# Optimization experiments

Hardware: AMD Instinct MI355X
Metric: run time of the kernel (lower is better)

Reference implementation:

```python
import jax, jax.numpy as jnp
import numpy as np
from jax import lax

B, C_IN, H_IN, W_IN = 128, 256, 8, 32
RH, RW = 16, 64            # rec-head resolution
YOH, XOH = RH // 2, RW // 2  # onehot sizes (8, 32)
HID = 256
NC = 163                   # num classes == embed size
T = 32                     # target length
C_ENC = C_IN + XOH + YOH   # 296 encoder channels
L = (RH // 2) * (RW // 2)  # 256 attention positions


def setup_inputs() -> dict:
    key = jax.random.key(0)
    ks = jax.random.split(key, 18)
    s = 0.05
    return {
        "x": jax.random.normal(ks[0], (B, C_IN, H_IN, W_IN), jnp.float32),
        "decoder_targets": jax.random.randint(ks[1], (B, T), 0, NC),
        "word_targets": jax.random.randint(ks[2], (B, T), 0, NC),
        # seq_encoder conv 3x3
        "conv_w": jax.random.normal(ks[3], (C_IN, C_IN, 3, 3), jnp.float32) * 0.02,
        "conv_b": jnp.zeros((C_IN,), jnp.float32),
        # decoder embedding (post kaiming re-init => random, not identity)
        "emb_dec": jax.random.normal(ks[4], (NC, NC), jnp.float32) * s,
        "word_w": jax.random.normal(ks[5], (HID, NC), jnp.float32) * s,
        "word_b": jnp.zeros((HID,), jnp.float32),
        "attn_w": jax.random.normal(ks[6], (HID, 2 * HID + XOH + YOH), jnp.float32) * s,
        "attn_b": jnp.zeros((HID,), jnp.float32),
        "attn_v": jax.random.normal(ks[7], (HID,), jnp.float32) * (1.0 / np.sqrt(HID)),
        # GRUCell, gate order [r, z, n]
        "gru_wih": jax.random.normal(ks[8], (3 * HID, 2 * HID + XOH + YOH), jnp.float32) * s,
        "gru_bih": jnp.zeros((3 * HID,), jnp.float32),
        "gru_whh": jax.random.normal(ks[9], (3 * HID, HID), jnp.float32) * s,
        "gru_bhh": jnp.zeros((3 * HID,), jnp.float32),
        "out_w": jax.random.normal(ks[10], (NC, HID), jnp.float32) * s,
        "out_b": jnp.zeros((NC,), jnp.float32),
        # positional one-hot embedding tables (also kaiming re-initialized)
        "x_emb": jax.random.normal(ks[11], (XOH, XOH), jnp.float32) * s,
        "y_emb": jax.random.normal(ks[12], (YOH, YOH), jnp.float32) * s,
    }


def _forward(x, conv_w, conv_b, emb_dec, word_w, word_b, attn_w, attn_b, attn_v,
             gru_wih, gru_bih, gru_whh, gru_bhh, out_w, out_b, x_emb, y_emb,
             decoder_targets, word_targets):
    b = x.shape[0]
    # rescale: bilinear upsample (align_corners=False ~ half-pixel)
    xr = jax.image.resize(x, (b, C_IN, RH, RW), method="linear")
    # seq_encoder: conv3x3 + ReLU + maxpool2
    conv = lax.conv_general_dilated(xr, conv_w, (1, 1), "SAME",
                                    dimension_numbers=("NCHW", "OIHW", "NCHW"))
    conv = jax.nn.relu(conv + conv_b[None, :, None, None])
    pooled = lax.reduce_window(conv, -jnp.inf, lax.max,
                               (1, 1, 2, 2), (1, 1, 2, 2), "VALID")  # (B,256,8,32)
    hf, wf = RH // 2, RW // 2
    # positional channels: x_map[c,y,x] = x_emb[x,c]; y_map[c,y,x] = y_emb[y,c]
    x_map = jnp.broadcast_to(x_emb.T[:, None, :], (XOH, hf, wf))
    y_map = jnp.broadcast_to(y_emb.T[:, :, None], (YOH, hf, wf))
    x_map = jnp.broadcast_to(x_map[None], (b, XOH, hf, wf))
    y_map = jnp.broadcast_to(y_map[None], (b, YOH, hf, wf))
    feat = jnp.concatenate([pooled, x_map, y_map], axis=1)      # (B,296,8,32)
    enc = feat.reshape(b, C_ENC, hf * wf).transpose(0, 2, 1)    # (B, L, C)

    t_len = decoder_targets.shape[1]
    # teacher forcing: input at step 0 is BOS (=0), else previous target
    inputs_seq = jnp.concatenate(
        [jnp.zeros((b, 1), decoder_targets.dtype), decoder_targets[:, :-1]], axis=1)

    def step(hidden, xs):
        tok, tgt = xs
        we = emb_dec[tok] @ word_w.T + word_b                   # (B, HID)
        # Bahdanau attention
        hrep = jnp.broadcast_to(hidden[:, None, :], (b, enc.shape[1], HID))
        cat = jnp.concatenate([hrep, enc], axis=-1)             # (B,L,2H+OH)
        energy = jnp.tanh(jnp.einsum("blc,hc->blh", cat, attn_w) + attn_b)
        scores = jnp.einsum("blh,h->bl", energy, attn_v)
        w = jax.nn.softmax(scores, axis=1)                      # (B,L)
        ctx = jnp.einsum("bl,blc->bc", w, enc)                  # (B, C)
        rin = jnp.concatenate([we, ctx], axis=-1)               # (B, 2H+OH)
        # GRUCell
        gi = rin @ gru_wih.T + gru_bih
        gh = hidden @ gru_whh.T + gru_bhh
        i_r, i_z, i_n = jnp.split(gi, 3, axis=-1)
        h_r, h_z, h_n = jnp.split(gh, 3, axis=-1)
        r = jax.nn.sigmoid(i_r + h_r)
        z = jax.nn.sigmoid(i_z + h_z)
        n = jnp.tanh(i_n + r * h_n)
        h_new = (1.0 - z) * n + z * hidden
        logp = jax.nn.log_softmax(h_new @ out_w.T + out_b, axis=1)
        # NLLLoss(ignore_index=-1, reduction='none')
        nll = -jnp.take_along_axis(logp, jnp.clip(tgt, 0)[:, None], axis=1)[:, 0]
        nll = jnp.where(tgt >= 0, nll, 0.0)
        return h_new, nll

    h0 = jnp.zeros((b, HID), jnp.float32)
    _, nlls = lax.scan(step, h0, (inputs_seq.T, word_targets.T))  # (T, B)
    loss_vec = nlls.sum(axis=0)                                   # (B,)
    return 0.2 * (loss_vec.sum() / loss_vec.shape[0])


def reference(x, decoder_targets, word_targets, conv_w, conv_b, emb_dec,
              word_w, word_b, attn_w, attn_b, attn_v, gru_wih, gru_bih,
              gru_whh, gru_bhh, out_w, out_b, x_emb, y_emb):
    return _forward(x, conv_w, conv_b, emb_dec, word_w, word_b, attn_w, attn_b,
                    attn_v, gru_wih, gru_bih, gru_whh, gru_bhh, out_w, out_b,
                    x_emb, y_emb, decoder_targets, word_targets)
```

## Files before the change

kernel.cpp:

```cpp
#include <hip/hip_runtime.h>
#include <hip/hip_bf16.h>
#include <math.h>

#define B    128
#define CIN  256
#define HIN  8
#define WIN_ 32
#define RH   16
#define RW   64
#define HID  256
#define NC   163
#define T    32
#define L    256
#define CENC 296

typedef __attribute__((ext_vector_type(8))) short short8;
typedef __attribute__((ext_vector_type(8))) unsigned short u16x8;
typedef __attribute__((ext_vector_type(4))) float f32x4;
typedef unsigned long long u64;

#define PH(k) ((((k) >> 3) * 12) + ((k) & 7))

__device__ __forceinline__ float bf2f(unsigned short u) {
    unsigned int x = ((unsigned int)u) << 16;
    return __uint_as_float(x);
}
__device__ __forceinline__ unsigned short f2bf(float f) {
    unsigned int x = __float_as_uint(f);
    unsigned int r = (x + 0x7FFFu + ((x >> 16) & 1u)) >> 16;
    return (unsigned short)r;
}
__device__ __forceinline__ float fast_tanh(float x) {
    float e = __expf(2.f * x);
    return 1.f - 2.f * __builtin_amdgcn_rcpf(e + 1.f);
}
__device__ __forceinline__ float fast_sigm(float x) {
    return __builtin_amdgcn_rcpf(1.f + __expf(-x));
}
__device__ __forceinline__ float wave_red_max(float v) {
    #pragma unroll
    for (int o = 32; o > 0; o >>= 1) v = fmaxf(v, __shfl_down(v, o, 64));
    return v;
}
__device__ __forceinline__ float wave_red_sum(float v) {
    #pragma unroll
    for (int o = 32; o > 0; o >>= 1) v += __shfl_down(v, o, 64);
    return v;
}
__device__ __forceinline__ float half_red_sum(float v) {
    #pragma unroll
    for (int o = 16; o > 0; o >>= 1) v += __shfl_down(v, o, 64);
    return v;
}

__global__ void __launch_bounds__(256) k_upsxt(const float* __restrict__ x,
                                               unsigned short* __restrict__ Xt) {
    __shared__ __align__(16) float sf[64 * 2 * 32];
    const int y = blockIdx.x;
    const int b = blockIdx.y;
    const int tid = threadIdx.x;
    float sy = 0.5f * y - 0.25f;
    int yq0 = (y - 1) >> 1;
    float wy = sy - (float)yq0;
    int y0c = min(max(yq0, 0), HIN - 1);
    int y1c = min(max(yq0 + 1, 0), HIN - 1);
    const int xo = tid & 63;
    const int cj = tid >> 6;
    float sx = 0.5f * xo - 0.25f;
    int xq0 = (xo - 1) >> 1;
    float wx = sx - (float)xq0;
    int x0c = min(max(xq0, 0), WIN_ - 1);
    int x1c = min(max(xq0 + 1, 0), WIN_ - 1);
    for (int cc = 0; cc < 4; cc++) {
        __syncthreads();
        #pragma unroll
        for (int i = 0; i < 4; i++) {
            int idx = tid * 4 + i;
            int c = idx >> 4;
            int rowh = (idx >> 3) & 1;
            int part = idx & 7;
            int ysrc = rowh ? y1c : y0c;
            float4 v = *reinterpret_cast<const float4*>(
                x + ((size_t)(b * CIN + cc * 64 + c) * HIN + ysrc) * WIN_ + part * 4);
            *reinterpret_cast<float4*>(sf + ((c * 2 + rowh) * 32 + part * 4)) = v;
        }
        __syncthreads();
        unsigned short ov[16];
        #pragma unroll
        for (int j = 0; j < 16; j++) {
            int c = cj * 16 + j;
            const float* r0 = sf + (c * 2 + 0) * 32;
            const float* r1 = sf + (c * 2 + 1) * 32;
            float v = (1.f - wy) * ((1.f - wx) * r0[x0c] + wx * r0[x1c])
                    +        wy  * ((1.f - wx) * r1[x0c] + wx * r1[x1c]);
            ov[j] = f2bf(v);
        }
        unsigned short* dst = Xt + ((size_t)((b * 16 + y) * 64 + xo)) * 256 + cc * 64 + cj * 16;
        *reinterpret_cast<u16x8*>(dst)     = *reinterpret_cast<u16x8*>(ov);
        *reinterpret_cast<u16x8*>(dst + 8) = *reinterpret_cast<u16x8*>(ov + 8);
    }
}

__global__ void k_wt(const float* __restrict__ conv_w, unsigned short* __restrict__ Wt) {
    int e = blockIdx.x * 256 + threadIdx.x;
    int ci = e & 255;
    int co = (e >> 8) & 255;
    int s  = e >> 16;
    Wt[(size_t)(s * 256 + co) * 256 + ci] = f2bf(conv_w[(size_t)(co * 256 + ci) * 9 + s]);
}

__global__ void __launch_bounds__(256) k_convmm(const unsigned short* __restrict__ Xt,
        const unsigned short* __restrict__ Wt, const float* __restrict__ conv_b,
        unsigned short* __restrict__ enc_bf) {
    __shared__ __align__(16) char smem[34048];
    unsigned short* A_s = (unsigned short*)smem;
    unsigned short* B_s = A_s + 128 * 40;
    float* pool = (float*)smem;
    const int mt = blockIdx.x;
    const int n0 = blockIdx.y * 128;
    const int b = mt >> 3;
    const int y0 = (mt & 7) * 2;
    const int tid = threadIdx.x;
    const int wave = tid >> 6, lane = tid & 63;
    const int mq = (wave & 1) * 64, nq = (wave >> 1) * 64;
    const int lm = lane & 15, lq = lane >> 4;
    f32x4 acc[4][4];
    #pragma unroll
    for (int mi = 0; mi < 4; mi++)
        #pragma unroll
        for (int ni = 0; ni < 4; ni++)
            #pragma unroll
            for (int r = 0; r < 4; r++) acc[mi][ni][r] = 0.f;

    for (int s9 = 0; s9 < 9; s9++) {
        const int ky = s9 / 3, kx = s9 % 3;
        const unsigned short* Wb = Wt + (size_t)s9 * 256 * 256;
        for (int kc = 0; kc < 256; kc += 32) {
            __syncthreads();
            #pragma unroll
            for (int it = 0; it < 2; it++) {
                int s2 = tid + it * 256;
                int pix = s2 >> 2, q4 = s2 & 3;
                int yy = y0 + (pix >> 6) + ky - 1;
                int xx = (pix & 63) + kx - 1;
                u16x8 va = {0, 0, 0, 0, 0, 0, 0, 0};
                if ((unsigned)yy < 16u && (unsigned)xx < 64u)
                    va = *reinterpret_cast<const u16x8*>(
                        Xt + ((size_t)((b * 16 + yy) * 64 + xx)) * 256 + kc + q4 * 8);
                *reinterpret_cast<u16x8*>(A_s + pix * 40 + q4 * 8) = va;
                u16x8 vb = *reinterpret_cast<const u16x8*>(
                    Wb + (size_t)(n0 + pix) * 256 + kc + q4 * 8);
                *reinterpret_cast<u16x8*>(B_s + pix * 40 + q4 * 8) = vb;
            }
            __syncthreads();
            short8 af[4], bfr[4];
            #pragma unroll
            for (int mi = 0; mi < 4; mi++)
                af[mi] = *reinterpret_cast<const short8*>(A_s + (mq + mi * 16 + lm) * 40 + lq * 8);
            #pragma unroll
            for (int ni = 0; ni < 4; ni++)
                bfr[ni] = *reinterpret_cast<const short8*>(B_s + (nq + ni * 16 + lm) * 40 + lq * 8);
            #pragma unroll
            for (int mi = 0; mi < 4; mi++)
                #pragma unroll
                for (int ni = 0; ni < 4; ni++)
                    acc[mi][ni] = __builtin_amdgcn_mfma_f32_16x16x32_bf16(
                        af[mi], bfr[ni], acc[mi][ni], 0, 0, 0);
        }
    }
    __syncthreads();
    #pragma unroll
    for (int mi = 0; mi < 4; mi++) {
        int px0 = mi * 8 + lq * 2;
        #pragma unroll
        for (int ni = 0; ni < 4; ni++) {
            int nl = nq + ni * 16 + lm;
            float pa = fmaxf(acc[mi][ni][0], acc[mi][ni][1]);
            float pb = fmaxf(acc[mi][ni][2], acc[mi][ni][3]);
            pool[((wave & 1) * 32 + px0) * 132 + nl] = pa;
            pool[((wave & 1) * 32 + px0 + 1) * 132 + nl] = pb;
        }
    }
    __syncthreads();
    {
        int base = tid * 16;
        int px = base >> 7;
        int nb = base & 127;
        unsigned short ov[16];
        #pragma unroll
        for (int i = 0; i < 16; i++) {
            int n = nb + i;
            float v = fmaxf(pool[px * 132 + n], pool[(32 + px) * 132 + n]) + conv_b[n0 + n];
            ov[i] = f2bf(fmaxf(v, 0.f));
        }
        unsigned short* dst = enc_bf + ((size_t)b * L + (mt & 7) * 32 + px) * CENC + n0 + nb;
        *reinterpret_cast<u16x8*>(dst)     = *reinterpret_cast<u16x8*>(ov);
        *reinterpret_cast<u16x8*>(dst + 8) = *reinterpret_cast<u16x8*>(ov + 8);
    }
}

__global__ void k_encpos(const float* __restrict__ x_emb, const float* __restrict__ y_emb,
                         unsigned short* __restrict__ enc_bf, unsigned short* __restrict__ pos2t) {
    int b = blockIdx.x, l = threadIdx.x;
    int yl = l >> 5, xl = l & 31;
    unsigned short* e = enc_bf + (size_t)(b * L + l) * CENC + 256;
    #pragma unroll
    for (int c = 0; c < 32; c++) e[c] = f2bf(x_emb[xl * 32 + c]);
    #pragma unroll
    for (int c = 0; c < 8; c++) e[32 + c] = f2bf(y_emb[yl * 8 + c]);
    if (b == 0) {
        #pragma unroll
        for (int c = 0; c < 32; c++) pos2t[c * 256 + l] = f2bf(x_emb[xl * 32 + c]);
        #pragma unroll
        for (int c = 0; c < 8; c++) pos2t[(32 + c) * 256 + l] = f2bf(y_emb[yl * 8 + c]);
    }
}

__global__ void __launch_bounds__(256) k_enct(const unsigned short* __restrict__ enc_bf,
                                              unsigned short* __restrict__ enc_t) {
    __shared__ unsigned short s[64 * 264];
    const int c0 = blockIdx.x * 64;
    const int b = blockIdx.y;
    const int tid = threadIdx.x;
    #pragma unroll
    for (int j = 0; j < 8; j++) {
        u16x8 u = *reinterpret_cast<const u16x8*>(
            enc_bf + ((size_t)b * L + tid) * CENC + c0 + j * 8);
        #pragma unroll
        for (int k = 0; k < 8; k++) s[(j * 8 + k) * 264 + tid] = u[k];
    }
    __syncthreads();
    {
        int c = tid >> 2, lp = tid & 3;
        const unsigned short* row = s + c * 264 + lp * 64;
        unsigned short* dst = enc_t + ((size_t)b * 256 + c0 + c) * L + lp * 64;
        #pragma unroll
        for (int i = 0; i < 8; i++)
            *reinterpret_cast<u16x8*>(dst + i * 8) =
                *reinterpret_cast<const u16x8*>(row + i * 8);
    }
}

__global__ void __launch_bounds__(256) k_etab(const float* __restrict__ emb_dec,
                                              const float* __restrict__ word_w,
                                              const float* __restrict__ word_b,
                                              float* __restrict__ E) {
    __shared__ float er[NC];
    int row = blockIdx.x, tid = threadIdx.x;
    for (int k = tid; k < NC; k += 256) er[k] = emb_dec[(size_t)row * NC + k];
    __syncthreads();
    float a = word_b[tid];
    for (int k = 0; k < NC; k++) a += er[k] * word_w[(size_t)tid * NC + k];
    E[(size_t)row * HID + tid] = a;
}

__global__ void k_prep(const float* __restrict__ attn_w, const float* __restrict__ out_w,
                       unsigned short* __restrict__ wA_bf, unsigned short* __restrict__ ow_bf) {
    int o = blockIdx.x, k = threadIdx.x;
    wA_bf[(size_t)o * 256 + k] = f2bf(attn_w[(size_t)o * 552 + k]);
    if (o < NC) ow_bf[(size_t)o * 256 + k] = f2bf(out_w[(size_t)o * 256 + k]);
}

__global__ void __launch_bounds__(1024) k_wpack(const float* __restrict__ wih,
        const float* __restrict__ whh, unsigned short* __restrict__ WpackC,
        unsigned short* __restrict__ WpackH) {
    const int blk = blockIdx.x;
    const int tid = threadIdx.x;
    unsigned short o[8];
    if (blk < 37) {
        #pragma unroll
        for (int j = 0; j < 8; j++) {
            int k = blk * 8 + j;
            float v = (tid < 768) ? wih[(size_t)tid * 552 + 256 + k] : 0.f;
            o[j] = f2bf(v);
        }
        *reinterpret_cast<u16x8*>(WpackC + ((size_t)blk * 1024 + tid) * 8) =
            *reinterpret_cast<u16x8*>(o);
    } else {
        int it = blk - 37;
        #pragma unroll
        for (int j = 0; j < 8; j++) {
            int k = it * 8 + j;
            float v = (tid < 768) ? whh[(size_t)tid * 256 + k] : 0.f;
            o[j] = f2bf(v);
        }
        *reinterpret_cast<u16x8*>(WpackH + ((size_t)it * 1024 + tid) * 8) =
            *reinterpret_cast<u16x8*>(o);
    }
}

__global__ void __launch_bounds__(768) k_wge(const float* __restrict__ wih,
                                             unsigned short* __restrict__ WgE) {
    int k = blockIdx.x, g = threadIdx.x;
    WgE[(size_t)k * 768 + g] = f2bf(wih[(size_t)g * 552 + k]);
}
__global__ void __launch_bounds__(768) k_gie(const float* __restrict__ E,
                                             const unsigned short* __restrict__ WgE,
                                             const float* __restrict__ bih,
                                             float* __restrict__ giE) {
    __shared__ float er[256];
    int v = blockIdx.x, g = threadIdx.x;
    if (g < 256) er[g] = E[(size_t)v * 256 + g];
    __syncthreads();
    float a = bih[g];
    #pragma unroll 4
    for (int k = 0; k < 256; k++) a += er[k] * bf2f(WgE[(size_t)k * 768 + g]);
    giE[(size_t)v * 768 + g] = a;
}

__global__ void __launch_bounds__(256) k_ep(const unsigned short* __restrict__ enc_bf,
                                            const float* __restrict__ attn_w,
                                            unsigned short* __restrict__ ep_t) {
    __shared__ __align__(16) float eS[16][132];
    __shared__ __align__(16) float wS[16][36];
    const int l0 = blockIdx.x * 128;
    const int h0 = blockIdx.y * 32;
    const int b = blockIdx.z;
    const int tid = threadIdx.x;
    const int hh = tid >> 5, ll = tid & 31;
    float acc[4][4];
    #pragma unroll
    for (int s2 = 0; s2 < 4; s2++)
        #pragma unroll
        for (int r = 0; r < 4; r++) acc[s2][r] = 0.f;
    for (int kc = 0; kc < CENC; kc += 16) {
        const int kn = min(16, CENC - kc);
        __syncthreads();
        #pragma unroll
        for (int it = 0; it < 2; it++) {
            int idx = it * 256 + tid;
            int lq = idx >> 2, kq = idx & 3;
            float v0 = 0.f, v1 = 0.f, v2 = 0.f, v3 = 0.f;
            if (kq * 4 < kn) {
                ushort4 u = *reinterpret_cast<const ushort4*>(
                    enc_bf + (size_t)(b * L + l0 + lq) * CENC + kc + kq * 4);
                v0 = bf2f(u.x); v1 = bf2f(u.y); v2 = bf2f(u.z); v3 = bf2f(u.w);
            }
            eS[kq * 4 + 0][lq] = v0; eS[kq * 4 + 1][lq] = v1;
            eS[kq * 4 + 2][lq] = v2; eS[kq * 4 + 3][lq] = v3;
        }
        if (tid < 128) {
            int hq = tid >> 2, kq = tid & 3;
            float4 v = make_float4(0.f, 0.f, 0.f, 0.f);
            if (kq * 4 < kn)
                v = *reinterpret_cast<const float4*>(attn_w + (size_t)(h0 + hq) * 552 + 256 + kc + kq * 4);
            wS[kq * 4 + 0][hq] = v.x; wS[kq * 4 + 1][hq] = v.y;
            wS[kq * 4 + 2][hq] = v.z; wS[kq * 4 + 3][hq] = v.w;
        }
        __syncthreads();
        #pragma unroll
        for (int k = 0; k < 16; k++) {
            float4 e = *reinterpret_cast<const float4*>(&eS[k][ll * 4]);
            float4 w = *reinterpret_cast<const float4*>(&wS[k][hh * 4]);
            float ev[4] = {e.x, e.y, e.z, e.w};
            float wv[4] = {w.x, w.y, w.z, w.w};
            #pragma unroll
            for (int s2 = 0; s2 < 4; s2++)
                #pragma unroll
                for (int r = 0; r < 4; r++) acc[s2][r] += wv[s2] * ev[r];
        }
    }
    #pragma unroll
    for (int r = 0; r < 4; r++) {
        ushort4 o;
        o.x = f2bf(acc[0][r]); o.y = f2bf(acc[1][r]);
        o.z = f2bf(acc[2][r]); o.w = f2bf(acc[3][r]);
        *reinterpret_cast<ushort4*>(
            ep_t + ((size_t)(b * L) + l0 + ll * 4 + r) * HID + h0 + hh * 4) = o;
    }
}

__global__ void k_init(u64* __restrict__ hX64, u64* __restrict__ sX64) {
    int gi = blockIdx.x * 256 + threadIdx.x;
    if (gi < B * 128) hX64[gi] = 0ull;
    else sX64[gi - B * 128] = 0ull;
}

__global__ void __launch_bounds__(1024) k_steps(
        const float* __restrict__ giE, const float* __restrict__ bhh,
        const unsigned short* __restrict__ ep_t, const unsigned short* __restrict__ enc_t,
        const unsigned short* __restrict__ wA_bf, const unsigned short* __restrict__ ow_bf,
        const unsigned short* __restrict__ pos2t,
        const unsigned short* __restrict__ WpackC, const unsigned short* __restrict__ WpackH,
        const float* __restrict__ attn_b, const float* __restrict__ attn_v,
        const float* __restrict__ out_b,
        const int* __restrict__ dec_tgt, const int* __restrict__ word_tgt,
        float* __restrict__ nllG,
        u64* __restrict__ hX64, u64* __restrict__ sX64) {
    const int bid = blockIdx.x;
    const bool roleA = bid < B;
    const int b = bid & (B - 1);
    const int tid = threadIdx.x;
    const int hwid = tid >> 5, l32 = tid & 31;

    __shared__ __align__(16) unsigned short big[L * 256];
    __shared__ __align__(16) unsigned short hmail[256];
    __shared__ __align__(16) unsigned short swl[256];
    __shared__ __align__(16) float rinF[552];
    __shared__ __align__(16) float hF[384];
    __shared__ __align__(16) float hpF[384], vbF[384], swlF[384];
    __shared__ float hfS[256];
    __shared__ float scr[256];
    __shared__ float red[16];
    __shared__ float rzS[512], inS[256], hnS[256];
    unsigned int* hmail32 = reinterpret_cast<unsigned int*>(hmail);
    unsigned int* swl32 = reinterpret_cast<unsigned int*>(swl);

    if (roleA) {
        if (tid < 256) vbF[PH(tid)] = attn_v[tid];
        {
            const u16x8* src = reinterpret_cast<const u16x8*>(ep_t + (size_t)b * L * 256);
            u16x8* dst = reinterpret_cast<u16x8*>(big);
            #pragma unroll
            for (int i = 0; i < 8; i++) dst[tid + i * 1024] = src[tid + i * 1024];
        }
        float nllacc = 0.f;
        __syncthreads();
        for (int t = 0; t <= T; t++) {
            if (tid < 128) {
                u64 want = (u64)(t + 1);
                u64 v;
                for (;;) {
                    v = __hip_atomic_load(&hX64[b * 128 + tid], __ATOMIC_RELAXED,
                                          __HIP_MEMORY_SCOPE_AGENT);
                    if ((v >> 32) == want) break;
                    __builtin_amdgcn_s_sleep(1);
                }
                unsigned int u = (unsigned int)v;
                hF[PH(2 * tid)]     = bf2f((unsigned short)(u & 0xffffu));
                hF[PH(2 * tid + 1)] = bf2f((unsigned short)(u >> 16));
            }
            __syncthreads();
            if (t < T) {
                {
                    float4 ha = *reinterpret_cast<const float4*>(hF + l32 * 12);
                    float4 hb = *reinterpret_cast<const float4*>(hF + l32 * 12 + 4);
                    #pragma unroll
                    for (int it = 0; it < 8; it++) {
                        int row = it * 32 + hwid;
                        u16x8 w = *reinterpret_cast<const u16x8*>(wA_bf + (size_t)row * 256 + l32 * 8);
                        float d = bf2f(w[0]) * ha.x + bf2f(w[1]) * ha.y
                                + bf2f(w[2]) * ha.z + bf2f(w[3]) * ha.w
                                + bf2f(w[4]) * hb.x + bf2f(w[5]) * hb.y
                                + bf2f(w[6]) * hb.z + bf2f(w[7]) * hb.w;
                        d = half_red_sum(d);
                        if (l32 == 0) hpF[PH(row)] = d + attn_b[row];
                    }
                }
                __syncthreads();
                {
                    float4 ha = *reinterpret_cast<const float4*>(hpF + l32 * 12);
                    float4 hb = *reinterpret_cast<const float4*>(hpF + l32 * 12 + 4);
                    float4 va = *reinterpret_cast<const float4*>(vbF + l32 * 12);
                    float4 vv = *reinterpret_cast<const float4*>(vbF + l32 * 12 + 4);
                    #pragma unroll
                    for (int it = 0; it < 8; it++) {
                        int row = it * 32 + hwid;
                        u16x8 e = *reinterpret_cast<const u16x8*>(big + (size_t)row * 256 + l32 * 8);
                        float d = va.x * fast_tanh(bf2f(e[0]) + ha.x)
                                + va.y * fast_tanh(bf2f(e[1]) + ha.y)
                                + va.z * fast_tanh(bf2f(e[2]) + ha.z)
                                + va.w * fast_tanh(bf2f(e[3]) + ha.w)
                                + vv.x * fast_tanh(bf2f(e[4]) + hb.x)
                                + vv.y * fast_tanh(bf2f(e[5]) + hb.y)
                                + vv.z * fast_tanh(bf2f(e[6]) + hb.z)
                                + vv.w * fast_tanh(bf2f(e[7]) + hb.w);
                        d = half_red_sum(d);
                        if (l32 == 0) scr[row] = d;
                    }
                }
                __syncthreads();
                float e2 = 0.f;
                if (tid < 256) {
                    e2 = __expf(scr[tid]);
                    float sm = wave_red_sum(e2);
                    if ((tid & 63) == 0) red[8 + (tid >> 6)] = sm;
                }
                __syncthreads();
                if (tid < 256) {
                    float invS = __builtin_amdgcn_rcpf(red[8] + red[9] + red[10] + red[11]);
                    swl[tid] = f2bf(e2 * invS);
                }
                __syncthreads();
                if (tid < 128)
                    __hip_atomic_store(&sX64[b * 128 + tid],
                                       ((u64)(t + 1) << 32) | (u64)swl32[tid],
                                       __ATOMIC_RELAXED, __HIP_MEMORY_SCOPE_AGENT);
            }
            if (t > 0) {
                float4 ha = *reinterpret_cast<const float4*>(hF + l32 * 12);
                float4 hb = *reinterpret_cast<const float4*>(hF + l32 * 12 + 4);
                #pragma unroll
                for (int it = 0; it < 6; it++) {
                    int row = it * 32 + hwid;
                    float d = 0.f;
                    if (row < NC) {
                        u16x8 w = *reinterpret_cast<const u16x8*>(ow_bf + (size_t)row * 256 + l32 * 8);
                        d = bf2f(w[0]) * ha.x + bf2f(w[1]) * ha.y
                          + bf2f(w[2]) * ha.z + bf2f(w[3]) * ha.w
                          + bf2f(w[4]) * hb.x + bf2f(w[5]) * hb.y
                          + bf2f(w[6]) * hb.z + bf2f(w[7]) * hb.w;
                    }
                    d = half_red_sum(d);
                    if (l32 == 0 && row < NC) scr[row] = d + out_b[row];
                }
                __syncthreads();
                float lg = -1e30f;
                if (tid < 256) {
                    if (tid < NC) lg = scr[tid];
                    float m = wave_red_max(lg);
                    if ((tid & 63) == 0) red[tid >> 6] = m;
                }
                __syncthreads();
                float M = fmaxf(fmaxf(red[0], red[1]), fmaxf(red[2], red[3]));
                if (tid < 256) {
                    float e = (tid < NC) ? __expf(lg - M) : 0.f;
                    float sm = wave_red_sum(e);
                    if ((tid & 63) == 0) red[8 + (tid >> 6)] = sm;
                }
                __syncthreads();
                if (tid == 0) {
                    float S = red[8] + red[9] + red[10] + red[11];
                    int tgt = word_tgt[b * T + (t - 1)];
                    if (tgt >= 0) nllacc += M + __logf(S) - scr[tgt];
                }
                __syncthreads();
            }
        }
        if (tid == 0) nllG[b] = nllacc;
    } else {
        {
            const u16x8* src = reinterpret_cast<const u16x8*>(enc_t + (size_t)b * 256 * 256);
            u16x8* dst = reinterpret_cast<u16x8*>(big);
            #pragma unroll
            for (int i = 0; i < 8; i++) dst[tid + i * 1024] = src[tid + i * 1024];
        }
        __syncthreads();
        for (int t = 0; t <= T; t++) {
            if (tid < 256) {
                float h;
                if (t == 0) {
                    h = 0.f;
                } else {
                    float hold = hfS[tid];
                    int tokp = (t == 1) ? 0 : dec_tgt[b * T + (t - 2)];
                    const float* gE = giE + (size_t)tokp * 768;
                    float r_ = fast_sigm(rzS[tid] + gE[tid] + bhh[tid]);
                    float z_ = fast_sigm(rzS[256 + tid] + gE[256 + tid] + bhh[256 + tid]);
                    float n_ = fast_tanh(inS[tid] + gE[512 + tid] + r_ * (hnS[tid] + bhh[512 + tid]));
                    h = (1.f - z_) * n_ + z_ * hold;
                }
                hfS[tid] = h;
                hmail[tid] = f2bf(h);
                rinF[296 + tid] = h;
            }
            __syncthreads();
            if (tid < 128)
                __hip_atomic_store(&hX64[b * 128 + tid],
                                   ((u64)(t + 1) << 32) | (u64)hmail32[tid],
                                   __ATOMIC_RELAXED, __HIP_MEMORY_SCOPE_AGENT);
            if (t == T) break;
            float hacc = 0.f;
            if (tid < 768) {
                float a0 = 0.f, a1 = 0.f;
                #pragma unroll 4
                for (int it = 0; it < 32; it++) {
                    u16x8 w = *reinterpret_cast<const u16x8*>(WpackH + ((size_t)it * 1024 + tid) * 8);
                    float4 ra = *reinterpret_cast<const float4*>(rinF + 296 + it * 8);
                    float4 rb = *reinterpret_cast<const float4*>(rinF + 296 + it * 8 + 4);
                    a0 += bf2f(w[0]) * ra.x + bf2f(w[2]) * ra.z
                        + bf2f(w[4]) * rb.x + bf2f(w[6]) * rb.z;
                    a1 += bf2f(w[1]) * ra.y + bf2f(w[3]) * ra.w
                        + bf2f(w[5]) * rb.y + bf2f(w[7]) * rb.w;
                }
                hacc = a0 + a1;
            }
            if (tid < 128) {
                u64 want = (u64)(t + 1);
                u64 v;
                for (;;) {
                    v = __hip_atomic_load(&sX64[b * 128 + tid], __ATOMIC_RELAXED,
                                          __HIP_MEMORY_SCOPE_AGENT);
                    if ((v >> 32) == want) break;
                    __builtin_amdgcn_s_sleep(1);
                }
                unsigned int u = (unsigned int)v;
                swlF[PH(2 * tid)]     = bf2f((unsigned short)(u & 0xffffu));
                swlF[PH(2 * tid + 1)] = bf2f((unsigned short)(u >> 16));
            }
            __syncthreads();
            {
                float4 sa = *reinterpret_cast<const float4*>(swlF + l32 * 12);
                float4 sb = *reinterpret_cast<const float4*>(swlF + l32 * 12 + 4);
                #pragma unroll
                for (int it = 0; it < 8; it++) {
                    int row = it * 32 + hwid;
                    u16x8 e = *reinterpret_cast<const u16x8*>(big + (size_t)row * 256 + l32 * 8);
                    float d = bf2f(e[0]) * sa.x + bf2f(e[1]) * sa.y
                            + bf2f(e[2]) * sa.z + bf2f(e[3]) * sa.w
                            + bf2f(e[4]) * sb.x + bf2f(e[5]) * sb.y
                            + bf2f(e[6]) * sb.z + bf2f(e[7]) * sb.w;
                    d = half_red_sum(d);
                    if (l32 == 0) rinF[row] = d;
                }
                #pragma unroll
                for (int it = 0; it < 2; it++) {
                    int row = it * 32 + hwid;
                    float d = 0.f;
                    if (row < 40) {
                        u16x8 p = *reinterpret_cast<const u16x8*>(pos2t + (size_t)row * 256 + l32 * 8);
                        d = bf2f(p[0]) * sa.x + bf2f(p[1]) * sa.y
                          + bf2f(p[2]) * sa.z + bf2f(p[3]) * sa.w
                          + bf2f(p[4]) * sb.x + bf2f(p[5]) * sb.y
                          + bf2f(p[6]) * sb.z + bf2f(p[7]) * sb.w;
                    }
                    d = half_red_sum(d);
                    if (l32 == 0 && row < 40) rinF[256 + row] = d;
                }
            }
            __syncthreads();
            if (tid < 768) {
                float c0 = 0.f, c1 = 0.f;
                #pragma unroll 4
                for (int it = 0; it < 37; it++) {
                    u16x8 w = *reinterpret_cast<const u16x8*>(WpackC + ((size_t)it * 1024 + tid) * 8);
                    float4 ra = *reinterpret_cast<const float4*>(rinF + it * 8);
                    float4 rb = *reinterpret_cast<const float4*>(rinF + it * 8 + 4);
                    c0 += bf2f(w[0]) * ra.x + bf2f(w[2]) * ra.z
                        + bf2f(w[4]) * rb.x + bf2f(w[6]) * rb.z;
                    c1 += bf2f(w[1]) * ra.y + bf2f(w[3]) * ra.w
                        + bf2f(w[5]) * rb.y + bf2f(w[7]) * rb.w;
                }
                float cacc = c0 + c1;
                if (tid < 512) rzS[tid] = cacc + hacc;
                else { inS[tid - 512] = cacc; hnS[tid - 512] = hacc; }
            }
            __syncthreads();
        }
    }
}

__global__ void k_reduce(const float* __restrict__ nll, float* __restrict__ out) {
    __shared__ float red[2];
    float v = nll[threadIdx.x];
    v = wave_red_sum(v);
    if ((threadIdx.x & 63) == 0) red[threadIdx.x >> 6] = v;
    __syncthreads();
    if (threadIdx.x == 0) out[0] = 0.2f * (red[0] + red[1]) * (1.f / 128.f);
}

extern "C" void kernel_launch(void* const* d_in, const int* in_sizes, int n_in,
                              void* d_out, int out_size, void* d_ws, size_t ws_size,
                              hipStream_t stream) {
    const float* x        = (const float*)d_in[0];
    const int*   dec_tgt  = (const int*)d_in[1];
    const int*   word_tgt = (const int*)d_in[2];
    const float* conv_w   = (const float*)d_in[3];
    const float* conv_b   = (const float*)d_in[4];
    const float* emb_dec  = (const float*)d_in[5];
    const float* word_w   = (const float*)d_in[6];
    const float* word_b   = (const float*)d_in[7];
    const float* attn_w   = (const float*)d_in[8];
    const float* attn_b   = (const float*)d_in[9];
    const float* attn_v   = (const float*)d_in[10];
    const float* gru_wih  = (const float*)d_in[11];
    const float* gru_bih  = (const float*)d_in[12];
    const float* gru_whh  = (const float*)d_in[13];
    const float* gru_bhh  = (const float*)d_in[14];
    const float* out_w    = (const float*)d_in[15];
    const float* out_b    = (const float*)d_in[16];
    const float* x_emb    = (const float*)d_in[17];
    const float* y_emb    = (const float*)d_in[18];

    char* ws = (char*)d_ws;
    size_t off = 0;
    auto alloc = [&](size_t bytes) -> void* {
        void* p = ws + off;
        off = (off + bytes + 255) & ~(size_t)255;
        return p;
    };
    unsigned short* Xt     = (unsigned short*)alloc((size_t)B * 16 * 64 * 256 * 2);
    unsigned short* enc_bf = (unsigned short*)alloc((size_t)B * L * CENC * 2);
    unsigned short* Wt     = (unsigned short*)alloc((size_t)9 * 256 * 256 * 2);
    float* E      = (float*)alloc((size_t)NC * HID * 4);
    unsigned short* wA_bf  = (unsigned short*)alloc((size_t)HID * HID * 2);
    unsigned short* ow_bf  = (unsigned short*)alloc((size_t)NC * HID * 2);
    unsigned short* WpackC = (unsigned short*)alloc((size_t)37 * 1024 * 8 * 2);
    unsigned short* WpackH = (unsigned short*)alloc((size_t)32 * 1024 * 8 * 2);
    unsigned short* WgE    = (unsigned short*)alloc((size_t)256 * 768 * 2);
    float* giE    = (float*)alloc((size_t)NC * 768 * 4);
    unsigned short* pos2t  = (unsigned short*)alloc((size_t)40 * 256 * 2);
    float* nllG   = (float*)alloc((size_t)B * 4);
    u64* hX64     = (u64*)alloc((size_t)B * 128 * 8);
    u64* sX64     = (u64*)alloc((size_t)B * 128 * 8);
    unsigned short* ep_t  = Xt;
    unsigned short* enc_t = Xt + (size_t)B * L * HID;
    float* out    = (float*)d_out;

    hipLaunchKernelGGL(k_init, dim3(128), dim3(256), 0, stream, hX64, sX64);
    hipLaunchKernelGGL(k_upsxt, dim3(16, 128), dim3(256), 0, stream, x, Xt);
    hipLaunchKernelGGL(k_wt, dim3(2304), dim3(256), 0, stream, conv_w, Wt);
    hipLaunchKernelGGL(k_encpos, dim3(128), dim3(256), 0, stream, x_emb, y_emb, enc_bf, pos2t);
    hipLaunchKernelGGL(k_convmm, dim3(1024, 2), dim3(256), 0, stream, Xt, Wt, conv_b, enc_bf);
    hipLaunchKernelGGL(k_etab, dim3(163), dim3(256), 0, stream, emb_dec, word_w, word_b, E);
    hipLaunchKernelGGL(k_prep, dim3(256), dim3(256), 0, stream, attn_w, out_w, wA_bf, ow_bf);
    hipLaunchKernelGGL(k_wpack, dim3(69), dim3(1024), 0, stream, gru_wih, gru_whh, WpackC, WpackH);
    hipLaunchKernelGGL(k_wge, dim3(256), dim3(768), 0, stream, gru_wih, WgE);
    hipLaunchKernelGGL(k_gie, dim3(163), dim3(768), 0, stream, E, WgE, gru_bih, giE);
    hipLaunchKernelGGL(k_ep, dim3(2, 8, 128), dim3(256), 0, stream, enc_bf, attn_w, ep_t);
    hipLaunchKernelGGL(k_enct, dim3(4, 128), dim3(256), 0, stream, enc_bf, enc_t);
    hipLaunchKernelGGL(k_steps, dim3(256), dim3(1024), 0, stream,
                       giE, gru_bhh, ep_t, enc_t, wA_bf, ow_bf, pos2t, WpackC, WpackH,
                       attn_b, attn_v, out_b, dec_tgt, word_tgt, nllG,
                       hX64, sX64);
    hipLaunchKernelGGL(k_reduce, dim3(1), dim3(128), 0, stream, nllG, out);
}
```

Before: 1.102 ms.

## Use MFMA for encoder attention projection and send fp32 mailbox values

Replaces the scalar FP32 encoder-projection GEMM (k_ep) with a bf16 MFMA tiled kernel that uses a pre-packed, zero-padded bf16 copy of the attention weight slice. It also changes the inter-block mailbox in the recurrent step kernel to carry one fp32 value per u64 slot instead of two packed bf16 values. Each lane now publishes directly, which removes the shared staging arrays and a __syncthreads per step. The cost is twice the mailbox slots and polling threads, and a small change in precision for the exchanged values.

```diff
diff --git a/kernel.cpp b/kernel.cpp
--- a/kernel.cpp
+++ b/kernel.cpp
@@ -255,10 +255,13 @@
 }
 
 __global__ void k_prep(const float* __restrict__ attn_w, const float* __restrict__ out_w,
-                       unsigned short* __restrict__ wA_bf, unsigned short* __restrict__ ow_bf) {
+                       unsigned short* __restrict__ wA_bf, unsigned short* __restrict__ ow_bf,
+                       unsigned short* __restrict__ wE_bf) {
     int o = blockIdx.x, k = threadIdx.x;
     wA_bf[(size_t)o * 256 + k] = f2bf(attn_w[(size_t)o * 552 + k]);
     if (o < NC) ow_bf[(size_t)o * 256 + k] = f2bf(out_w[(size_t)o * 256 + k]);
+    for (int k2 = k; k2 < 320; k2 += 256)
+        wE_bf[(size_t)o * 320 + k2] = (k2 < 296) ? f2bf(attn_w[(size_t)o * 552 + 256 + k2]) : 0;
 }
 
 __global__ void __launch_bounds__(1024) k_wpack(const float* __restrict__ wih,
@@ -308,72 +311,73 @@
     giE[(size_t)v * 768 + g] = a;
 }
 
-__global__ void __launch_bounds__(256) k_ep(const unsigned short* __restrict__ enc_bf,
-                                            const float* __restrict__ attn_w,
-                                            unsigned short* __restrict__ ep_t) {
-    __shared__ __align__(16) float eS[16][132];
-    __shared__ __align__(16) float wS[16][36];
-    const int l0 = blockIdx.x * 128;
-    const int h0 = blockIdx.y * 32;
-    const int b = blockIdx.z;
+__global__ void __launch_bounds__(256) k_epmm(const unsigned short* __restrict__ enc_bf,
+        const unsigned short* __restrict__ wE_bf, unsigned short* __restrict__ ep_t) {
+    __shared__ __align__(16) unsigned short A_s[128 * 40];
+    __shared__ __align__(16) unsigned short B_s[128 * 40];
+    const int mt = blockIdx.x;
+    const int b = blockIdx.y;
+    const int l0 = (mt & 1) * 128;
+    const int n0 = (mt >> 1) * 128;
     const int tid = threadIdx.x;
-    const int hh = tid >> 5, ll = tid & 31;
-    float acc[4][4];
-    #pragma unroll
-    for (int s2 = 0; s2 < 4; s2++)
-        #pragma unroll
-        for (int r = 0; r < 4; r++) acc[s2][r] = 0.f;
-    for (int kc = 0; kc < CENC; kc += 16) {
-        const int kn = min(16, CENC - kc);
+    const int wave = tid >> 6, lane = tid & 63;
+    const int mq = (wave & 1) * 64, nq = (wave >> 1) * 64;
+    const int lm = lane & 15, lq = lane >> 4;
+    f32x4 acc[4][4];
+    #pragma unroll
+    for (int mi = 0; mi < 4; mi++)
+        #pragma unroll
+        for (int ni = 0; ni < 4; ni++)
+            #pragma unroll
+            for (int r = 0; r < 4; r++) acc[mi][ni][r] = 0.f;
+
+    for (int kc = 0; kc < 320; kc += 32) {
         __syncthreads();
         #pragma unroll
         for (int it = 0; it < 2; it++) {
-            int idx = it * 256 + tid;
-            int lq = idx >> 2, kq = idx & 3;
-            float v0 = 0.f, v1 = 0.f, v2 = 0.f, v3 = 0.f;
-            if (kq * 4 < kn) {
-                ushort4 u = *reinterpret_cast<const ushort4*>(
-                    enc_bf + (size_t)(b * L + l0 + lq) * CENC + kc + kq * 4);
-                v0 = bf2f(u.x); v1 = bf2f(u.y); v2 = bf2f(u.z); v3 = bf2f(u.w);
-            }
-            eS[kq * 4 + 0][lq] = v0; eS[kq * 4 + 1][lq] = v1;
-            eS[kq * 4 + 2][lq] = v2; eS[kq * 4 + 3][lq] = v3;
-        }
-        if (tid < 128) {
-            int hq = tid >> 2, kq = tid & 3;
-            float4 v = make_float4(0.f, 0.f, 0.f, 0.f);
-            if (kq * 4 < kn)
-                v = *reinterpret_cast<const float4*>(attn_w + (size_t)(h0 + hq) * 552 + 256 + kc + kq * 4);
-            wS[kq * 4 + 0][hq] = v.x; wS[kq * 4 + 1][hq] = v.y;
-            wS[kq * 4 + 2][hq] = v.z; wS[kq * 4 + 3][hq] = v.w;
+            int s2 = tid + it * 256;
+            int row = s2 >> 2, q4 = s2 & 3;
+            int k = kc + q4 * 8;
+            u16x8 va = {0, 0, 0, 0, 0, 0, 0, 0};
+            if (k < 296)
+                va = *reinterpret_cast<const u16x8*>(
+                    enc_bf + (size_t)(b * L + l0 + row) * CENC + k);
+            *reinterpret_cast<u16x8*>(A_s + row * 40 + q4 * 8) = va;
+            u16x8 vb = *reinterpret_cast<const u16x8*>(
+                wE_bf + (size_t)(n0 + row) * 320 + k);
+            *reinterpret_cast<u16x8*>(B_s + row * 40 + q4 * 8) = vb;
         }
         __syncthreads();
-        #pragma unroll
-        for (int k = 0; k < 16; k++) {
-            float4 e = *reinterpret_cast<const float4*>(&eS[k][ll * 4]);
-            float4 w = *reinterpret_cast<const float4*>(&wS[k][hh * 4]);
-            float ev[4] = {e.x, e.y, e.z, e.w};
-            float wv[4] = {w.x, w.y, w.z, w.w};
-            #pragma unroll
-            for (int s2 = 0; s2 < 4; s2++)
-                #pragma unroll
-                for (int r = 0; r < 4; r++) acc[s2][r] += wv[s2] * ev[r];
-        }
-    }
-    #pragma unroll
-    for (int r = 0; r < 4; r++) {
-        ushort4 o;
-        o.x = f2bf(acc[0][r]); o.y = f2bf(acc[1][r]);
-        o.z = f2bf(acc[2][r]); o.w = f2bf(acc[3][r]);
-        *reinterpret_cast<ushort4*>(
-            ep_t + ((size_t)(b * L) + l0 + ll * 4 + r) * HID + h0 + hh * 4) = o;
-    }
+        short8 af[4], bfr[4];
+        #pragma unroll
+        for (int mi = 0; mi < 4; mi++)
+            af[mi] = *reinterpret_cast<const short8*>(A_s + (mq + mi * 16 + lm) * 40 + lq * 8);
+        #pragma unroll
+        for (int ni = 0; ni < 4; ni++)
+            bfr[ni] = *reinterpret_cast<const short8*>(B_s + (nq + ni * 16 + lm) * 40 + lq * 8);
+        #pragma unroll
+        for (int mi = 0; mi < 4; mi++)
+            #pragma unroll
+            for (int ni = 0; ni < 4; ni++)
+                acc[mi][ni] = __builtin_amdgcn_mfma_f32_16x16x32_bf16(
+                    af[mi], bfr[ni], acc[mi][ni], 0, 0, 0);
+    }
+    #pragma unroll
+    for (int mi = 0; mi < 4; mi++)
+        #pragma unroll
+        for (int ni = 0; ni < 4; ni++)
+            #pragma unroll
+            for (int r = 0; r < 4; r++) {
+                int l = l0 + mq + mi * 16 + lq * 4 + r;
+                int h = n0 + nq + ni * 16 + lm;
+                ep_t[((size_t)b * L + l) * HID + h] = f2bf(acc[mi][ni][r]);
+            }
 }
 
 __global__ void k_init(u64* __restrict__ hX64, u64* __restrict__ sX64) {
     int gi = blockIdx.x * 256 + threadIdx.x;
-    if (gi < B * 128) hX64[gi] = 0ull;
-    else sX64[gi - B * 128] = 0ull;
+    if (gi < B * 256) hX64[gi] = 0ull;
+    else sX64[gi - B * 256] = 0ull;
 }
 
 __global__ void __launch_bounds__(1024) k_steps(
@@ -394,8 +398,6 @@
     const int hwid = tid >> 5, l32 = tid & 31;
 
     __shared__ __align__(16) unsigned short big[L * 256];
-    __shared__ __align__(16) unsigned short hmail[256];
-    __shared__ __align__(16) unsigned short swl[256];
     __shared__ __align__(16) float rinF[552];
     __shared__ __align__(16) float hF[384];
     __shared__ __align__(16) float hpF[384], vbF[384], swlF[384];
@@ -403,8 +405,6 @@
     __shared__ float scr[256];
     __shared__ float red[16];
     __shared__ float rzS[512], inS[256], hnS[256];
-    unsigned int* hmail32 = reinterpret_cast<unsigned int*>(hmail);
-    unsigned int* swl32 = reinterpret_cast<unsigned int*>(swl);
 
     if (roleA) {
         if (tid < 256) vbF[PH(tid)] = attn_v[tid];
@@ -417,18 +417,16 @@
         float nllacc = 0.f;
         __syncthreads();
         for (int t = 0; t <= T; t++) {
-            if (tid < 128) {
+            if (tid < 256) {
                 u64 want = (u64)(t + 1);
                 u64 v;
                 for (;;) {
-                    v = __hip_atomic_load(&hX64[b * 128 + tid], __ATOMIC_RELAXED,
+                    v = __hip_atomic_load(&hX64[b * 256 + tid], __ATOMIC_RELAXED,
                                           __HIP_MEMORY_SCOPE_AGENT);
                     if ((v >> 32) == want) break;
                     __builtin_amdgcn_s_sleep(1);
                 }
-                unsigned int u = (unsigned int)v;
-                hF[PH(2 * tid)]     = bf2f((unsigned short)(u & 0xffffu));
-                hF[PH(2 * tid + 1)] = bf2f((unsigned short)(u >> 16));
+                hF[PH(tid)] = __uint_as_float((unsigned int)v);
             }
             __syncthreads();
             if (t < T) {
@@ -479,13 +477,11 @@
                 __syncthreads();
                 if (tid < 256) {
                     float invS = __builtin_amdgcn_rcpf(red[8] + red[9] + red[10] + red[11]);
-                    swl[tid] = f2bf(e2 * invS);
-                }
-                __syncthreads();
-                if (tid < 128)
-                    __hip_atomic_store(&sX64[b * 128 + tid],
-                                       ((u64)(t + 1) << 32) | (u64)swl32[tid],
+                    float wv = e2 * invS;
+                    __hip_atomic_store(&sX64[b * 256 + tid],
+                                       ((u64)(t + 1) << 32) | (u64)__float_as_uint(wv),
                                        __ATOMIC_RELAXED, __HIP_MEMORY_SCOPE_AGENT);
+                }
             }
             if (t > 0) {
                 float4 ha = *reinterpret_cast<const float4*>(hF + l32 * 12);
@@ -550,15 +546,13 @@
                     float n_ = fast_tanh(inS[tid] + gE[512 + tid] + r_ * (hnS[tid] + bhh[512 + tid]));
                     h = (1.f - z_) * n_ + z_ * hold;
                 }
+                __hip_atomic_store(&hX64[b * 256 + tid],
+                                   ((u64)(t + 1) << 32) | (u64)__float_as_uint(h),
+                                   __ATOMIC_RELAXED, __HIP_MEMORY_SCOPE_AGENT);
                 hfS[tid] = h;
-                hmail[tid] = f2bf(h);
                 rinF[296 + tid] = h;
             }
             __syncthreads();
-            if (tid < 128)
-                __hip_atomic_store(&hX64[b * 128 + tid],
-                                   ((u64)(t + 1) << 32) | (u64)hmail32[tid],
-                                   __ATOMIC_RELAXED, __HIP_MEMORY_SCOPE_AGENT);
             if (t == T) break;
             float hacc = 0.f;
             if (tid < 768) {
@@ -575,18 +569,16 @@
                 }
                 hacc = a0 + a1;
             }
-            if (tid < 128) {
+            if (tid < 256) {
                 u64 want = (u64)(t + 1);
                 u64 v;
                 for (;;) {
-                    v = __hip_atomic_load(&sX64[b * 128 + tid], __ATOMIC_RELAXED,
+                    v = __hip_atomic_load(&sX64[b * 256 + tid], __ATOMIC_RELAXED,
                                           __HIP_MEMORY_SCOPE_AGENT);
                     if ((v >> 32) == want) break;
                     __builtin_amdgcn_s_sleep(1);
                 }
-                unsigned int u = (unsigned int)v;
-                swlF[PH(2 * tid)]     = bf2f((unsigned short)(u & 0xffffu));
-                swlF[PH(2 * tid + 1)] = bf2f((unsigned short)(u >> 16));
+                swlF[PH(tid)] = __uint_as_float((unsigned int)v);
             }
             __syncthreads();
             {
@@ -685,29 +677,30 @@
     float* E      = (float*)alloc((size_t)NC * HID * 4);
     unsigned short* wA_bf  = (unsigned short*)alloc((size_t)HID * HID * 2);
     unsigned short* ow_bf  = (unsigned short*)alloc((size_t)NC * HID * 2);
+    unsigned short* wE_bf  = (unsigned short*)alloc((size_t)HID * 320 * 2);
     unsigned short* WpackC = (unsigned short*)alloc((size_t)37 * 1024 * 8 * 2);
     unsigned short* WpackH = (unsigned short*)alloc((size_t)32 * 1024 * 8 * 2);
     unsigned short* WgE    = (unsigned short*)alloc((size_t)256 * 768 * 2);
     float* giE    = (float*)alloc((size_t)NC * 768 * 4);
     unsigned short* pos2t  = (unsigned short*)alloc((size_t)40 * 256 * 2);
     float* nllG   = (float*)alloc((size_t)B * 4);
-    u64* hX64     = (u64*)alloc((size_t)B * 128 * 8);
-    u64* sX64     = (u64*)alloc((size_t)B * 128 * 8);
+    u64* hX64     = (u64*)alloc((size_t)B * 256 * 8);
+    u64* sX64     = (u64*)alloc((size_t)B * 256 * 8);
     unsigned short* ep_t  = Xt;
     unsigned short* enc_t = Xt + (size_t)B * L * HID;
     float* out    = (float*)d_out;
 
-    hipLaunchKernelGGL(k_init, dim3(128), dim3(256), 0, stream, hX64, sX64);
+    hipLaunchKernelGGL(k_init, dim3(256), dim3(256), 0, stream, hX64, sX64);
     hipLaunchKernelGGL(k_upsxt, dim3(16, 128), dim3(256), 0, stream, x, Xt);
     hipLaunchKernelGGL(k_wt, dim3(2304), dim3(256), 0, stream, conv_w, Wt);
     hipLaunchKernelGGL(k_encpos, dim3(128), dim3(256), 0, stream, x_emb, y_emb, enc_bf, pos2t);
     hipLaunchKernelGGL(k_convmm, dim3(1024, 2), dim3(256), 0, stream, Xt, Wt, conv_b, enc_bf);
     hipLaunchKernelGGL(k_etab, dim3(163), dim3(256), 0, stream, emb_dec, word_w, word_b, E);
-    hipLaunchKernelGGL(k_prep, dim3(256), dim3(256), 0, stream, attn_w, out_w, wA_bf, ow_bf);
+    hipLaunchKernelGGL(k_prep, dim3(256), dim3(256), 0, stream, attn_w, out_w, wA_bf, ow_bf, wE_bf);
     hipLaunchKernelGGL(k_wpack, dim3(69), dim3(1024), 0, stream, gru_wih, gru_whh, WpackC, WpackH);
     hipLaunchKernelGGL(k_wge, dim3(256), dim3(768), 0, stream, gru_wih, WgE);
     hipLaunchKernelGGL(k_gie, dim3(163), dim3(768), 0, stream, E, WgE, gru_bih, giE);
-    hipLaunchKernelGGL(k_ep, dim3(2, 8, 128), dim3(256), 0, stream, enc_bf, attn_w, ep_t);
+    hipLaunchKernelGGL(k_epmm, dim3(4, 128), dim3(256), 0, stream, enc_bf, wE_bf, ep_t);
     hipLaunchKernelGGL(k_enct, dim3(4, 128), dim3(256), 0, stream, enc_bf, enc_t);
     hipLaunchKernelGGL(k_steps, dim3(256), dim3(1024), 0, stream,
                        giE, gru_bhh, ep_t, enc_t, wA_bf, ow_bf, pos2t, WpackC, WpackH,
```

Result: faster. 1.058 ms (-4.1%).
